# Performance work log

Hardware: AMD Instinct MI355X
Metric: run time of the kernel (lower is better)

## Reference

```python
import jax, jax.numpy as jnp
import numpy as np

R = 12          # resolution (H = W = G); L = R**3 = 1728
HEADS = 12


def setup_inputs() -> dict:
    key = jax.random.key(0)
    k1, k2, k3 = jax.random.split(key, 3)
    B, L, C = 4, R ** 3, 768
    qkv = jax.random.normal(k1, (3, B, L, C), dtype=jnp.float32)
    lepe_w = jax.random.normal(k2, (C, 1, 3, 3, 3), dtype=jnp.float32) * 0.05
    lepe_b = jax.random.normal(k3, (C,), dtype=jnp.float32) * 0.01
    return {"qkv": qkv, "lepe_w": lepe_w, "lepe_b": lepe_b}


def reference(qkv, lepe_w, lepe_b):
    # qkv: [3, B, L, C]; idx=0 => window == full volume, so attention is dense over L.
    q, k, v = qkv[0], qkv[1], qkv[2]
    B, L, C = q.shape
    hd = C // HEADS
    scale = hd ** -0.5

    # im2cswin with full-volume window preserves token order: [B, L, C] -> [B, H, L, d]
    qh = q.reshape(B, L, HEADS, hd).transpose(0, 2, 1, 3)
    kh = k.reshape(B, L, HEADS, hd).transpose(0, 2, 1, 3)

    # get_lepe: v -> [B, C, R, R, R], depthwise 3x3x3 conv (groups=C)
    v_img = v.transpose(0, 2, 1).reshape(B, C, R, R, R)
    lepe = jax.lax.conv_general_dilated(
        v_img, lepe_w, window_strides=(1, 1, 1), padding="SAME",
        dimension_numbers=("NCDHW", "OIDHW", "NCDHW"), feature_group_count=C,
    ) + lepe_b[None, :, None, None, None]
    lepe = lepe.reshape(B, HEADS, hd, L).transpose(0, 1, 3, 2)   # [B, H, L, d]
    vh = v_img.reshape(B, HEADS, hd, L).transpose(0, 1, 3, 2)    # [B, H, L, d]

    attn = jax.nn.softmax(jnp.einsum("bhqd,bhkd->bhqk", qh * scale, kh), axis=-1)
    out = jnp.einsum("bhqk,bhkd->bhqd", attn, vh) + lepe          # [B, H, L, d]

    # windows2img with full window is an inverse reshape back to [B, L, C]
    return out.transpose(0, 2, 1, 3).reshape(B, L, C)
```

## Files before the change

### kernel.cpp

```cpp
#include <hip/hip_runtime.h>

#define RR 12
#define LL 1728
#define CC 768
#define HEADS 12
#define HD 64
#define BATCH 4

typedef __attribute__((ext_vector_type(8))) short bf8;
typedef __attribute__((ext_vector_type(4))) float f4;

__device__ inline unsigned short f2bf(float x) {
  unsigned int u = __float_as_uint(x);
  return (unsigned short)((u + 0x7FFFu + ((u >> 16) & 1u)) >> 16);
}
__device__ inline unsigned short f2bfr(float x) {
  return (unsigned short)((__float_as_uint(x) + 0x8000u) >> 16);
}

__device__ inline float fast_exp2(float x) {
#if __has_builtin(__builtin_amdgcn_exp2f)
  return __builtin_amdgcn_exp2f(x);
#else
  return exp2f(x);
#endif
}

__device__ inline void gld16(const unsigned short* g, unsigned short* l) {
  __builtin_amdgcn_global_load_lds((const __attribute__((address_space(1))) unsigned int*)g,
                                   (__attribute__((address_space(3))) unsigned int*)l, 16, 0, 0);
}

#define QSCALE 0.1803368801111244f

#define NLEPE 5184
#define NPREP 1296

__global__ __launch_bounds__(256) void combined_kernel(const float* __restrict__ qkv,
                                                       const float* __restrict__ w,
                                                       const float* __restrict__ bias,
                                                       unsigned short* __restrict__ qb,
                                                       unsigned short* __restrict__ kb,
                                                       unsigned short* __restrict__ vT,
                                                       float* __restrict__ out) {
  __shared__ __align__(16) unsigned char smem[27648];
  const int bid = blockIdx.x;
  const int t = threadIdx.x;

  if (bid < NLEPE) {
    const int xg = (bid % 3) * 4;
    const int line = (bid / 3) % 144;
    const int ct = (bid / 432) % 3;
    const int b = bid / 1296;
    const int z = line / RR;
    const int y = line % RR;
    const int c0 = ct * 256;
    const int c = c0 + t;
    float* w_lds = (float*)smem;

    {
      const float* wsrc = w + (size_t)c0 * 27;
#pragma unroll
      for (int i = 0; i < 7; ++i) {
        const int idx = i * 256 + t;
        if (idx < 1728) *(float4*)&w_lds[idx * 4] = *(const float4*)&wsrc[idx * 4];
      }
    }
    __syncthreads();
    float wreg[27];
#pragma unroll
    for (int j = 0; j < 27; ++j) wreg[j] = w_lds[t * 27 + j];

    const float* vb = qkv + ((size_t)(2 * BATCH + b)) * LL * CC + c;
    const float bv = bias[c];
    float acc[4] = {bv, bv, bv, bv};

#pragma unroll
    for (int dz = -1; dz <= 1; ++dz) {
#pragma unroll
      for (int dy = -1; dy <= 1; ++dy) {
        const int zz = z + dz, yy = y + dy;
        const bool lineok = ((unsigned)zz < RR) & ((unsigned)yy < RR);
        const int base = (zz * RR + yy) * RR;
        float v6[6];
#pragma unroll
        for (int p = 0; p < 6; ++p) {
          const int xx = xg - 1 + p;
          const bool ok = lineok & ((unsigned)xx < RR);
          const int lp = ok ? base + xx : 0;
          const float vv = vb[(size_t)lp * CC];
          v6[p] = ok ? vv : 0.f;
        }
        const int jb = ((dz + 1) * 3 + (dy + 1)) * 3;
        const float wL = wreg[jb], wC = wreg[jb + 1], wR = wreg[jb + 2];
#pragma unroll
        for (int i = 0; i < 4; ++i)
          acc[i] += wL * v6[i] + wC * v6[i + 1] + wR * v6[i + 2];
      }
    }
    const size_t obase = ((size_t)b * LL + line * RR + xg) * CC + c;
#pragma unroll
    for (int i = 0; i < 4; ++i) out[obase + (size_t)i * CC] = acc[i];

  } else {
    const int p = bid - NLEPE;
    const int lt = p % 27;
    const int h = (p / 27) % HEADS;
    const int b = p / (27 * HEADS);
    unsigned short* tl = (unsigned short*)smem;

    {
      const int r0 = t >> 4;
      const int c4 = (t & 15) * 4;
#pragma unroll
      for (int pi = 0; pi < 4; ++pi) {
        const int row = lt * 64 + pi * 16 + r0;
        const size_t off = ((size_t)b * LL + row) * CC + h * HD + c4;
        const float4 qv = *(const float4*)(qkv + off);
        ushort4 oq;
        oq.x = f2bf(qv.x * QSCALE); oq.y = f2bf(qv.y * QSCALE);
        oq.z = f2bf(qv.z * QSCALE); oq.w = f2bf(qv.w * QSCALE);
        *(ushort4*)(qb + off) = oq;
        const float4 kv = *(const float4*)(qkv + (size_t)BATCH * LL * CC + off);
        ushort4 ok;
        ok.x = f2bf(kv.x); ok.y = f2bf(kv.y); ok.z = f2bf(kv.z); ok.w = f2bf(kv.w);
        *(ushort4*)(kb + off) = ok;
      }
    }

    const float* vsrc = qkv + ((size_t)(2 * BATCH + b)) * LL * CC;
#pragma unroll
    for (int it = 0; it < 4; ++it) {
      const int idx = it * 256 + t;
      const int lrow = idx >> 4;
      const int c4 = (idx & 15) * 4;
      const float4 vv = *(const float4*)(vsrc + (size_t)(lt * 64 + lrow) * CC + h * HD + c4);
      tl[(c4 + 0) * 65 + lrow] = f2bf(vv.x);
      tl[(c4 + 1) * 65 + lrow] = f2bf(vv.y);
      tl[(c4 + 2) * 65 + lrow] = f2bf(vv.z);
      tl[(c4 + 3) * 65 + lrow] = f2bf(vv.w);
    }
    __syncthreads();
#pragma unroll
    for (int it = 0; it < 4; ++it) {
      const int idx = it * 256 + t;
      const int drow = idx >> 4;
      const int u = idx & 15;
      const int s4 = u * 4;
      const int kbase = (((u >> 3) * 2 + (u & 1)) << 4) + (((u >> 1) & 3) << 2);
      ushort4 o;
      o.x = tl[drow * 65 + kbase + 0];
      o.y = tl[drow * 65 + kbase + 1];
      o.z = tl[drow * 65 + kbase + 2];
      o.w = tl[drow * 65 + kbase + 3];
      *(ushort4*)(vT + (((size_t)(b * HEADS + h) * HD + drow) * LL) + lt * 64 + s4) = o;
    }
  }
}

__global__ __launch_bounds__(256) void attn_kernel(const unsigned short* __restrict__ qb,
                                                   const unsigned short* __restrict__ kb,
                                                   const unsigned short* __restrict__ vT,
                                                   float* __restrict__ out) {
  __shared__ unsigned short k_lds[2][64 * 64];
  __shared__ unsigned short v_lds[2][64 * 64];

  const int qt = blockIdx.x;
  const int h = blockIdx.y;
  const int b = blockIdx.z;
  const int t = threadIdx.x;
  const int lane = t & 63;
  const int wave = t >> 6;
  const int m = lane & 15;
  const int quad = lane >> 4;

  bf8 qf[2];
  {
    const size_t qbase = ((size_t)(b * LL + qt * 64 + wave * 16 + m)) * CC + h * HD;
    qf[0] = *(const bf8*)(qb + qbase + quad * 8);
    qf[1] = *(const bf8*)(qb + qbase + 32 + quad * 8);
  }

  int koff[2], voff[2], ldsb[2];
#pragma unroll
  for (int j = 0; j < 2; ++j) {
    const int cidx = (j * 4 + wave) * 64 + lane;
    const int row = cidx >> 3;
    const int sc = (cidx & 7) ^ (row & 7);
    koff[j] = row * CC + sc * 8;
    voff[j] = row * LL + sc * 8;
    ldsb[j] = (j * 4 + wave) * 512;
  }

  const unsigned short* kgb = kb + (size_t)b * LL * CC + h * HD;
  const unsigned short* vgb = vT + ((size_t)(b * HEADS + h) * HD) * LL;

  gld16(kgb + koff[0], &k_lds[0][ldsb[0]]);
  gld16(kgb + koff[1], &k_lds[0][ldsb[1]]);
  gld16(vgb + voff[0], &v_lds[0][ldsb[0]]);
  gld16(vgb + voff[1], &v_lds[0][ldsb[1]]);

  f4 o_acc[4] = {};
  float psum = 0.f;

#define ATTN_BODY(KT, CUR)                                                              \
  {                                                                                     \
    __syncthreads();            \
    if ((KT) < 26) {                                                                    \
      const size_t ko = (size_t)((KT) + 1) * 64 * CC;                                   \
      const int vo = ((KT) + 1) * 64;                                                   \
      gld16(kgb + ko + koff[0], &k_lds[(CUR) ^ 1][ldsb[0]]);                            \
      gld16(kgb + ko + koff[1], &k_lds[(CUR) ^ 1][ldsb[1]]);                            \
      gld16(vgb + vo + voff[0], &v_lds[(CUR) ^ 1][ldsb[0]]);                            \
      gld16(vgb + vo + voff[1], &v_lds[(CUR) ^ 1][ldsb[1]]);                            \
    }                                                                                   \
    f4 s_acc[4] = {};                                                                   \
    _Pragma("unroll")                                                                   \
    for (int nt = 0; nt < 4; ++nt) {                                                    \
      _Pragma("unroll")                                                                 \
      for (int ks = 0; ks < 2; ++ks) {                                                  \
        const int cc = ((ks * 4 + quad) ^ (m & 7)) * 8;                                 \
        const bf8 kf = *(const bf8*)&k_lds[CUR][(nt * 16 + m) * 64 + cc];               \
        s_acc[nt] = __builtin_amdgcn_mfma_f32_16x16x32_bf16(kf, qf[ks], s_acc[nt], 0, 0, 0); \
      }                                                                                 \
    }                                                                                   \
    bf8 pf[2];                                                                          \
    _Pragma("unroll")                                                                   \
    for (int ks = 0; ks < 2; ++ks) {                                                    \
      union { bf8 v; unsigned int w[4]; } pu;                                           \
      _Pragma("unroll")                                                                 \
      for (int bb = 0; bb < 2; ++bb) {                                                  \
        const int nt = ks * 2 + bb;                                                     \
        const float p0 = fast_exp2(s_acc[nt][0]);                                       \
        const float p1 = fast_exp2(s_acc[nt][1]);                                       \
        const float p2 = fast_exp2(s_acc[nt][2]);                                       \
        const float p3 = fast_exp2(s_acc[nt][3]);                                       \
        psum += (p0 + p1) + (p2 + p3);                                                  \
        pu.w[bb * 2 + 0] = (unsigned int)f2bfr(p0) | ((unsigned int)f2bfr(p1) << 16);   \
        pu.w[bb * 2 + 1] = (unsigned int)f2bfr(p2) | ((unsigned int)f2bfr(p3) << 16);   \
      }                                                                                 \
      pf[ks] = pu.v;                                                                    \
    }                                                                                   \
    _Pragma("unroll")                                                                   \
    for (int nt = 0; nt < 4; ++nt) {                                                    \
      _Pragma("unroll")                                                                 \
      for (int ks = 0; ks < 2; ++ks) {                                                  \
        const int cc = ((ks * 4 + quad) ^ (m & 7)) * 8;                                 \
        const bf8 vf = *(const bf8*)&v_lds[CUR][(nt * 16 + m) * 64 + cc];               \
        o_acc[nt] = __builtin_amdgcn_mfma_f32_16x16x32_bf16(vf, pf[ks], o_acc[nt], 0, 0, 0); \
      }                                                                                 \
    }                                                                                   \
  }

  for (int ktp = 0; ktp < 13; ++ktp) {
    const int kt0 = ktp * 2;
    ATTN_BODY(kt0, 0)
    ATTN_BODY(kt0 + 1, 1)
  }
  ATTN_BODY(26, 0)
#undef ATTN_BODY

  float s = psum;
  s += __shfl_xor(s, 16);
  s += __shfl_xor(s, 32);
  const float inv = 1.0f / s;
  const int rowq = qt * 64 + wave * 16 + m;
  float* op = out + ((size_t)b * LL + rowq) * CC + h * HD + quad * 4;
#pragma unroll
  for (int nt = 0; nt < 4; ++nt) {
    float4 o4 = *(float4*)&op[nt * 16];
    o4.x += o_acc[nt][0] * inv;
    o4.y += o_acc[nt][1] * inv;
    o4.z += o_acc[nt][2] * inv;
    o4.w += o_acc[nt][3] * inv;
    *(float4*)&op[nt * 16] = o4;
  }
}

extern "C" void kernel_launch(void* const* d_in, const int* in_sizes, int n_in,
                              void* d_out, int out_size, void* d_ws, size_t ws_size,
                              hipStream_t stream) {
  (void)in_sizes; (void)n_in; (void)ws_size; (void)out_size;
  const float* qkv = (const float*)d_in[0];
  const float* lepe_w = (const float*)d_in[1];
  const float* lepe_b = (const float*)d_in[2];
  float* out = (float*)d_out;

  const size_t NE = (size_t)BATCH * LL * CC;
  unsigned short* qb = (unsigned short*)d_ws;
  unsigned short* kb = qb + NE;
  unsigned short* vT = kb + NE;

  combined_kernel<<<dim3(NLEPE + NPREP), 256, 0, stream>>>(qkv, lepe_w, lepe_b, qb, kb, vT, out);
  attn_kernel<<<dim3(27, HEADS, BATCH), 256, 0, stream>>>(qb, kb, vT, out);
}
```

Measured before the change: 193.1 us.

## Restructure attention into 512-thread blocks with triple-buffered staggered K/V pipeline

```diff
diff --git a/kernel.cpp b/kernel.cpp
--- a/kernel.cpp
+++ b/kernel.cpp
@@ -33,7 +33,7 @@
 
 #define QSCALE 0.1803368801111244f
 
-#define NLEPE 5184
+#define NLEPE 1728
 #define NPREP 1296
 
 __global__ __launch_bounds__(256) void combined_kernel(const float* __restrict__ qkv,
@@ -48,10 +48,9 @@
   const int t = threadIdx.x;
 
   if (bid < NLEPE) {
-    const int xg = (bid % 3) * 4;
-    const int line = (bid / 3) % 144;
-    const int ct = (bid / 432) % 3;
-    const int b = bid / 1296;
+    const int line = bid % 144;
+    const int ct = (bid / 144) % 3;
+    const int b = bid / 432;
     const int z = line / RR;
     const int y = line % RR;
     const int c0 = ct * 256;
@@ -73,7 +72,9 @@
 
     const float* vb = qkv + ((size_t)(2 * BATCH + b)) * LL * CC + c;
     const float bv = bias[c];
-    float acc[4] = {bv, bv, bv, bv};
+    float acc[RR];
+#pragma unroll
+    for (int i = 0; i < RR; ++i) acc[i] = bv;
 
 #pragma unroll
     for (int dz = -1; dz <= 1; ++dz) {
@@ -82,25 +83,25 @@
         const int zz = z + dz, yy = y + dy;
         const bool lineok = ((unsigned)zz < RR) & ((unsigned)yy < RR);
         const int base = (zz * RR + yy) * RR;
-        float v6[6];
-#pragma unroll
-        for (int p = 0; p < 6; ++p) {
-          const int xx = xg - 1 + p;
+        float v14[RR + 2];
+#pragma unroll
+        for (int p = 0; p < RR + 2; ++p) {
+          const int xx = p - 1;
           const bool ok = lineok & ((unsigned)xx < RR);
           const int lp = ok ? base + xx : 0;
           const float vv = vb[(size_t)lp * CC];
-          v6[p] = ok ? vv : 0.f;
+          v14[p] = ok ? vv : 0.f;
         }
         const int jb = ((dz + 1) * 3 + (dy + 1)) * 3;
         const float wL = wreg[jb], wC = wreg[jb + 1], wR = wreg[jb + 2];
 #pragma unroll
-        for (int i = 0; i < 4; ++i)
-          acc[i] += wL * v6[i] + wC * v6[i + 1] + wR * v6[i + 2];
+        for (int i = 0; i < RR; ++i)
+          acc[i] += wL * v14[i] + wC * v14[i + 1] + wR * v14[i + 2];
       }
     }
-    const size_t obase = ((size_t)b * LL + line * RR + xg) * CC + c;
-#pragma unroll
-    for (int i = 0; i < 4; ++i) out[obase + (size_t)i * CC] = acc[i];
+    const size_t obase = ((size_t)b * LL + line * RR) * CC + c;
+#pragma unroll
+    for (int i = 0; i < RR; ++i) out[obase + (size_t)i * CC] = acc[i];
 
   } else {
     const int p = bid - NLEPE;
@@ -158,16 +159,22 @@
   }
 }
 
-__global__ __launch_bounds__(256) void attn_kernel(const unsigned short* __restrict__ qb,
-                                                   const unsigned short* __restrict__ kb,
-                                                   const unsigned short* __restrict__ vT,
-                                                   float* __restrict__ out) {
-  __shared__ unsigned short k_lds[2][64 * 64];
-  __shared__ unsigned short v_lds[2][64 * 64];
-
-  const int qt = blockIdx.x;
-  const int h = blockIdx.y;
-  const int b = blockIdx.z;
+__global__ __launch_bounds__(512, 6) void attn_kernel(const unsigned short* __restrict__ qb,
+                                                      const unsigned short* __restrict__ kb,
+                                                      const unsigned short* __restrict__ vT,
+                                                      float* __restrict__ out) {
+  __shared__ unsigned short k_lds[3][64 * 64];
+  __shared__ unsigned short v_lds[3][64 * 64];
+
+  const int g = blockIdx.x;
+  const int xcd = g & 7;
+  const int ix = g >> 3;
+  const int qt = ix % 14;
+  const int bh = xcd * 6 + ix / 14;
+  const int h = bh % HEADS;
+  const int b = bh / HEADS;
+  const int stg = (qt * 2) % 27;
+
   const int t = threadIdx.x;
   const int lane = t & 63;
   const int wave = t >> 6;
@@ -176,54 +183,61 @@
 
   bf8 qf[2];
   {
-    const size_t qbase = ((size_t)(b * LL + qt * 64 + wave * 16 + m)) * CC + h * HD;
+    int row = qt * 128 + wave * 16 + m;
+    row = row < LL ? row : LL - 1;
+    const size_t qbase = ((size_t)(b * LL + row)) * CC + h * HD;
     qf[0] = *(const bf8*)(qb + qbase + quad * 8);
     qf[1] = *(const bf8*)(qb + qbase + 32 + quad * 8);
   }
 
-  int koff[2], voff[2], ldsb[2];
-#pragma unroll
-  for (int j = 0; j < 2; ++j) {
-    const int cidx = (j * 4 + wave) * 64 + lane;
+  int koff, voff, ldsb;
+  {
+    const int cidx = wave * 64 + lane;
     const int row = cidx >> 3;
     const int sc = (cidx & 7) ^ (row & 7);
-    koff[j] = row * CC + sc * 8;
-    voff[j] = row * LL + sc * 8;
-    ldsb[j] = (j * 4 + wave) * 512;
+    koff = row * CC + sc * 8;
+    voff = row * LL + sc * 8;
+    ldsb = wave * 512;
   }
 
   const unsigned short* kgb = kb + (size_t)b * LL * CC + h * HD;
   const unsigned short* vgb = vT + ((size_t)(b * HEADS + h) * HD) * LL;
 
-  gld16(kgb + koff[0], &k_lds[0][ldsb[0]]);
-  gld16(kgb + koff[1], &k_lds[0][ldsb[1]]);
-  gld16(vgb + voff[0], &v_lds[0][ldsb[0]]);
-  gld16(vgb + voff[1], &v_lds[0][ldsb[1]]);
+#define ISSUE_TILE(KT, BUF)                                                             \
+  {                                                                                     \
+    gld16(kgb + (size_t)(KT) * (64 * CC) + koff, &k_lds[BUF][ldsb]);                    \
+    gld16(vgb + (KT) * 64 + voff, &v_lds[BUF][ldsb]);                                   \
+  }
+
+  ISSUE_TILE(stg, 0)
+  {
+    int k1 = stg + 1; if (k1 >= 27) k1 -= 27;
+    ISSUE_TILE(k1, 1)
+  }
 
   f4 o_acc[4] = {};
   float psum = 0.f;
 
-#define ATTN_BODY(KT, CUR)                                                              \
+#define ATTN_BODY(I, STG, WAITN, DOISSUE)                                               \
   {                                                                                     \
-    __syncthreads();            \
-    if ((KT) < 26) {                                                                    \
-      const size_t ko = (size_t)((KT) + 1) * 64 * CC;                                   \
-      const int vo = ((KT) + 1) * 64;                                                   \
-      gld16(kgb + ko + koff[0], &k_lds[(CUR) ^ 1][ldsb[0]]);                            \
-      gld16(kgb + ko + koff[1], &k_lds[(CUR) ^ 1][ldsb[1]]);                            \
-      gld16(vgb + vo + voff[0], &v_lds[(CUR) ^ 1][ldsb[0]]);                            \
-      gld16(vgb + vo + voff[1], &v_lds[(CUR) ^ 1][ldsb[1]]);                            \
+    __asm__ volatile("s_waitcnt vmcnt(" #WAITN ")" ::: "memory");                       \
+    __builtin_amdgcn_s_barrier();                                                       \
+    if (DOISSUE) {                                                                      \
+      int ktn = stg + (I) + 2; if (ktn >= 27) ktn -= 27;                                \
+      ISSUE_TILE(ktn, ((STG) + 2) % 3)                                                  \
     }                                                                                   \
     f4 s_acc[4] = {};                                                                   \
+    __builtin_amdgcn_s_setprio(1);                                                      \
     _Pragma("unroll")                                                                   \
     for (int nt = 0; nt < 4; ++nt) {                                                    \
       _Pragma("unroll")                                                                 \
       for (int ks = 0; ks < 2; ++ks) {                                                  \
         const int cc = ((ks * 4 + quad) ^ (m & 7)) * 8;                                 \
-        const bf8 kf = *(const bf8*)&k_lds[CUR][(nt * 16 + m) * 64 + cc];               \
+        const bf8 kf = *(const bf8*)&k_lds[STG][(nt * 16 + m) * 64 + cc];               \
         s_acc[nt] = __builtin_amdgcn_mfma_f32_16x16x32_bf16(kf, qf[ks], s_acc[nt], 0, 0, 0); \
       }                                                                                 \
     }                                                                                   \
+    __builtin_amdgcn_s_setprio(0);                                                      \
     bf8 pf[2];                                                                          \
     _Pragma("unroll")                                                                   \
     for (int ks = 0; ks < 2; ++ks) {                                                    \
@@ -241,39 +255,47 @@
       }                                                                                 \
       pf[ks] = pu.v;                                                                    \
     }                                                                                   \
+    __builtin_amdgcn_s_setprio(1);                                                      \
     _Pragma("unroll")                                                                   \
     for (int nt = 0; nt < 4; ++nt) {                                                    \
       _Pragma("unroll")                                                                 \
       for (int ks = 0; ks < 2; ++ks) {                                                  \
         const int cc = ((ks * 4 + quad) ^ (m & 7)) * 8;                                 \
-        const bf8 vf = *(const bf8*)&v_lds[CUR][(nt * 16 + m) * 64 + cc];               \
+        const bf8 vf = *(const bf8*)&v_lds[STG][(nt * 16 + m) * 64 + cc];               \
         o_acc[nt] = __builtin_amdgcn_mfma_f32_16x16x32_bf16(vf, pf[ks], o_acc[nt], 0, 0, 0); \
       }                                                                                 \
     }                                                                                   \
-  }
-
-  for (int ktp = 0; ktp < 13; ++ktp) {
-    const int kt0 = ktp * 2;
-    ATTN_BODY(kt0, 0)
-    ATTN_BODY(kt0 + 1, 1)
-  }
-  ATTN_BODY(26, 0)
+    __builtin_amdgcn_s_setprio(0);                                                      \
+  }
+
+  for (int ip = 0; ip < 8; ++ip) {
+    const int i0 = ip * 3;
+    ATTN_BODY(i0 + 0, 0, 2, true)
+    ATTN_BODY(i0 + 1, 1, 2, true)
+    ATTN_BODY(i0 + 2, 2, 2, true)
+  }
+  ATTN_BODY(24, 0, 2, true)
+  ATTN_BODY(25, 1, 2, false)
+  ATTN_BODY(26, 2, 0, false)
 #undef ATTN_BODY
+#undef ISSUE_TILE
 
   float s = psum;
   s += __shfl_xor(s, 16);
   s += __shfl_xor(s, 32);
   const float inv = 1.0f / s;
-  const int rowq = qt * 64 + wave * 16 + m;
-  float* op = out + ((size_t)b * LL + rowq) * CC + h * HD + quad * 4;
-#pragma unroll
-  for (int nt = 0; nt < 4; ++nt) {
-    float4 o4 = *(float4*)&op[nt * 16];
-    o4.x += o_acc[nt][0] * inv;
-    o4.y += o_acc[nt][1] * inv;
-    o4.z += o_acc[nt][2] * inv;
-    o4.w += o_acc[nt][3] * inv;
-    *(float4*)&op[nt * 16] = o4;
+  const int rowq = qt * 128 + wave * 16 + m;
+  if (rowq < LL) {
+    float* op = out + ((size_t)b * LL + rowq) * CC + h * HD + quad * 4;
+#pragma unroll
+    for (int nt = 0; nt < 4; ++nt) {
+      float4 o4 = *(float4*)&op[nt * 16];
+      o4.x += o_acc[nt][0] * inv;
+      o4.y += o_acc[nt][1] * inv;
+      o4.z += o_acc[nt][2] * inv;
+      o4.w += o_acc[nt][3] * inv;
+      *(float4*)&op[nt * 16] = o4;
+    }
   }
 }
 
@@ -292,5 +314,5 @@
   unsigned short* vT = kb + NE;
 
   combined_kernel<<<dim3(NLEPE + NPREP), 256, 0, stream>>>(qkv, lepe_w, lepe_b, qb, kb, vT, out);
-  attn_kernel<<<dim3(27, HEADS, BATCH), 256, 0, stream>>>(qb, kb, vT, out);
-}
+  attn_kernel<<<dim3(672), 512, 0, stream>>>(qb, kb, vT, out);
+}
```

Result: faster. 181.1 us (-6.2%).
